# Optimization experiments

Measured on AMD Instinct MI355X. Metric: run time of the kernel, lower is better.

## Reference

```python
import jax, jax.numpy as jnp
import numpy as np

B, S, D, H, DK, F = 8, 1024, 1024, 16, 64, 4096
EPS = 1e-5


def _layer_norm(x, g, b):
    mu = jnp.mean(x, axis=-1, keepdims=True)
    var = jnp.var(x, axis=-1, keepdims=True)
    return (x - mu) * jax.lax.rsqrt(var + EPS) * g + b


def setup_inputs() -> dict:
    key = jax.random.key(0)
    ks = jax.random.split(key, 16)
    s = lambda fan: 1.0 / np.sqrt(fan)
    return {
        "src": jax.random.normal(ks[0], (B, S, D), dtype=jnp.float32),
        "Wq": jax.random.uniform(ks[1], (H, D, DK), jnp.float32, -s(D), s(D)),
        "bq": jnp.zeros((H, DK), jnp.float32),
        "Wk": jax.random.uniform(ks[2], (H, D, DK), jnp.float32, -s(D), s(D)),
        "bk": jnp.zeros((H, DK), jnp.float32),
        "Wv": jax.random.uniform(ks[3], (H, D, DK), jnp.float32, -s(D), s(D)),
        "bv": jnp.zeros((H, DK), jnp.float32),
        "Wo": jax.random.uniform(ks[4], (H * DK, D), jnp.float32, -s(H * DK), s(H * DK)),
        "bo": jnp.zeros((D,), jnp.float32),
        "g1": jnp.ones((D,), jnp.float32),
        "be1": jnp.zeros((D,), jnp.float32),
        "W1": jax.random.uniform(ks[5], (D, F), jnp.float32, -s(D), s(D)),
        "b1": jnp.zeros((F,), jnp.float32),
        "W2": jax.random.uniform(ks[6], (F, D), jnp.float32, -s(F), s(F)),
        "b2": jnp.zeros((D,), jnp.float32),
        "g2": jnp.ones((D,), jnp.float32),
        "be2": jnp.zeros((D,), jnp.float32),
    }


def reference(src, Wq, bq, Wk, bk, Wv, bv, Wo, bo, g1, be1, W1, b1, W2, b2, g2, be2):
    # Per-head projections (vectorized over the Python head loop of the original)
    q = jnp.einsum("bsd,hdk->bhsk", src, Wq) + bq[:, None, :]
    k = jnp.einsum("bsd,hdk->bhsk", src, Wk) + bk[:, None, :]
    v = jnp.einsum("bsd,hdk->bhsk", src, Wv) + bv[:, None, :]
    scale = 1.0 / jnp.sqrt(jnp.asarray(DK, src.dtype))
    scores = jnp.einsum("bhsk,bhtk->bhst", q, k) * scale  # [B,H,S,S]
    attn = jax.nn.softmax(scores, axis=-1)
    o = jnp.einsum("bhst,bhtk->bhsk", attn, v)
    # torch.cat over heads on last dim -> [B,S,H*DK] with head-major feature order
    o = o.transpose(0, 2, 1, 3).reshape(B, S, H * DK)
    attn_out = o @ Wo + bo
    x = _layer_norm(src + attn_out, g1, be1)  # dropout inactive at inference
    ff = jax.nn.relu(x @ W1 + b1) @ W2 + b2
    return _layer_norm(x + ff, g2, be2)
```

## Files before the change

### kernel.cpp

```cpp
#include <hip/hip_runtime.h>

#define Bq 8
#define Sq 1024
#define Dq 1024
#define Hq 16
#define DKq 64
#define Fq 4096
#define TOK (Bq*Sq)

typedef unsigned short u16;
typedef unsigned int u32;
typedef __bf16 bf16x8 __attribute__((ext_vector_type(8)));
typedef float  f32x4  __attribute__((ext_vector_type(4)));

__device__ __forceinline__ float bf2f(u16 u) {
  u32 x = ((u32)u) << 16;
  float f; __builtin_memcpy(&f, &x, 4); return f;
}
__device__ __forceinline__ u16 f2bf(float f) {
  u32 u; __builtin_memcpy(&u, &f, 4);
  u += 0x7fffu + ((u >> 16) & 1u);
  return (u16)(u >> 16);
}
__device__ __forceinline__ void async16(const u16* g, u16* l) {
  __builtin_amdgcn_global_load_lds(
      (__attribute__((address_space(1))) void*)(g),
      (__attribute__((address_space(3))) void*)(l), 16, 0, 0);
}
__device__ __forceinline__ u16 load_in(const void* p, long idx, u32 fp32) {
  return fp32 ? f2bf(((const float*)p)[idx]) : ((const u16*)p)[idx];
}

struct InTab { const void* p[17]; int n[17]; };

__global__ void detect_all(InTab tab, u32* flags) {
  __shared__ int sh[3][256];
  int bi = blockIdx.x;
  const u16* buf = (const u16*)tab.p[bi];
  long n = tab.n[bi];
  long m = n < 65536 ? n : 65536;
  int t = threadIdx.x;
  int nanpat = 0, evz = 0, oddnz = 0;
  for (long i = t; i < m; i += 256) {
    u16 v = buf[i];
    if ((v & 0x7F80u) == 0x7F80u) nanpat++;
    if ((i & 1) == 0) { if (v == 0) evz++; }
    else { if (v != 0) oddnz++; }
  }
  sh[0][t] = nanpat; sh[1][t] = evz; sh[2][t] = oddnz;
  __syncthreads();
  for (int s = 128; s > 0; s >>= 1) {
    if (t < s) { sh[0][t] += sh[0][t+s]; sh[1][t] += sh[1][t+s]; sh[2][t] += sh[2][t+s]; }
    __syncthreads();
  }
  if (t == 0) {
    long half = m / 2;
    bool fp32 = (sh[0][0] > 8) ||
                (sh[1][0] > (half * 9) / 10 && sh[2][0] > (half * 9) / 10);
    flags[bi] = fp32 ? 1u : 0u;
  }
}

__global__ void diag_ws_too_small(u16* out, float code) { out[0] = f2bf(code); }

__global__ void diag_mixed(const u32* flags, void* out) {
  u32 a = flags[0];
  if (flags[1] != a || flags[7] != a || flags[11] != a || flags[13] != a) {
    if (a) ((float*)out)[0] = 3000.0f;
    else ((u16*)out)[0] = f2bf(3000.0f);
  }
}

__global__ __launch_bounds__(256) void pack_all(const void* __restrict__ Wq,
                                                const void* __restrict__ Wk,
                                                const void* __restrict__ Wv,
                                                const void* __restrict__ Wo,
                                                const void* __restrict__ W1,
                                                const void* __restrict__ W2,
                                                u16* __restrict__ Wqkv_t,
                                                u16* __restrict__ Wo_t,
                                                u16* __restrict__ W1_t,
                                                u16* __restrict__ W2_t,
                                                const u32* __restrict__ flags) {
  int id = blockIdx.x;
  const void* in; u16* out; u32 f; int R, C; long zin; int r0, c0;
  if (id < 768) {
    int w = id >> 8, t = id & 255;
    int z = t >> 4, xt = t & 15;
    in = (w == 0) ? Wq : ((w == 1) ? Wk : Wv);
    f = flags[(w == 0) ? 1 : ((w == 1) ? 3 : 5)];
    R = 1024; C = 64;
    zin = (long)z * 65536;
    out = Wqkv_t + (long)w * 1048576 + (long)z * 65536;
    r0 = xt * 64; c0 = 0;
  } else if (id < 1024) {
    int t = id - 768; int xt = t & 15, yt = t >> 4;
    in = Wo; f = flags[7]; R = 1024; C = 1024; zin = 0; out = Wo_t;
    r0 = xt * 64; c0 = yt * 64;
  } else if (id < 2048) {
    int t = id - 1024; int xt = t & 15, yt = t >> 4;
    in = W1; f = flags[11]; R = 1024; C = 4096; zin = 0; out = W1_t;
    r0 = xt * 64; c0 = yt * 64;
  } else {
    int t = id - 2048; int xt = t & 63, yt = t >> 6;
    in = W2; f = flags[13]; R = 4096; C = 1024; zin = 0; out = W2_t;
    r0 = xt * 64; c0 = yt * 64;
  }
  __shared__ u16 tile[64][65];
  int tx = threadIdx.x & 63, ty = threadIdx.x >> 6;
#pragma unroll
  for (int it = 0; it < 16; it++) {
    int row = it * 4 + ty;
    tile[row][tx] = load_in(in, zin + (long)(r0 + row) * C + (c0 + tx), f);
  }
  __syncthreads();
#pragma unroll
  for (int it = 0; it < 16; it++) {
    int cc = it * 4 + ty;
    out[(long)(c0 + cc) * R + r0 + tx] = tile[tx][cc];
  }
}

struct CvtTab { const void* p[10]; int flagidx[10]; int dstoff[10]; int n[10]; };
__global__ void cvt_small(CvtTab tab, u16* __restrict__ dst, const u32* __restrict__ flags) {
  int e = blockIdx.x;
  u32 f = flags[tab.flagidx[e]];
  const void* p = tab.p[e];
  int n = tab.n[e], o = tab.dstoff[e];
  for (int i = threadIdx.x; i < n; i += 256) dst[o + i] = load_in(p, i, f);
}

__global__ __launch_bounds__(256) void cvt_src(const void* __restrict__ in,
                                               u16* __restrict__ out,
                                               const u32* __restrict__ flag) {
  u32 f = *flag;
  long i8 = ((long)blockIdx.x * 256 + threadIdx.x) * 8;
  if (f) {
    const float4* f4 = (const float4*)((const float*)in + i8);
    float4 a = f4[0], b = f4[1];
    u16 v[8] = {f2bf(a.x), f2bf(a.y), f2bf(a.z), f2bf(a.w),
                f2bf(b.x), f2bf(b.y), f2bf(b.z), f2bf(b.w)};
    *(uint4*)(out + i8) = *(const uint4*)v;
  } else {
    *(uint4*)(out + i8) = *(const uint4*)((const u16*)in + i8);
  }
}

__global__ __launch_bounds__(256) void gemm_bt(const u16* __restrict__ A,
                                               const u16* __restrict__ Bt,
                                               const u16* __restrict__ bias,
                                               u16* __restrict__ C,
                                               int M, int N, int K, int act) {
  __shared__ alignas(16) u16 sA[2][128 * 32];
  __shared__ alignas(16) u16 sB[2][128 * 32];
  const int tid = threadIdx.x;
  const int wv = tid >> 6, lane = tid & 63;
  const int m16 = lane & 15, quad = lane >> 4;
  const long bm = (long)blockIdx.x * 128;
  const long bn = (long)blockIdx.y * 128;
  const int wm = (wv >> 1) * 64, wn = (wv & 1) * 64;

  f32x4 acc[4][4];
#pragma unroll
  for (int i = 0; i < 4; i++)
#pragma unroll
    for (int j = 0; j < 4; j++) acc[i][j] = (f32x4){0.f, 0.f, 0.f, 0.f};

  const int row_s = tid >> 2;
  const int col_s = (tid & 3) * 8;
  const u16* gA0 = A + (bm + row_s) * (long)K + col_s;
  const u16* gA1 = gA0 + 64 * (long)K;
  const u16* gB0 = Bt + (bn + row_s) * (long)K + col_s;
  const u16* gB1 = gB0 + 64 * (long)K;

  auto stage = [&](int p, int k) {
    async16(gA0 + k, &sA[p][wv * 512]);
    async16(gA1 + k, &sA[p][2048 + wv * 512]);
    async16(gB0 + k, &sB[p][wv * 512]);
    async16(gB1 + k, &sB[p][2048 + wv * 512]);
  };
  auto compute = [&](int p) {
    bf16x8 af[4], bf_[4];
#pragma unroll
    for (int mi = 0; mi < 4; mi++)
      af[mi] = *(const bf16x8*)&sA[p][(wm + mi * 16 + m16) * 32 + quad * 8];
#pragma unroll
    for (int ni = 0; ni < 4; ni++)
      bf_[ni] = *(const bf16x8*)&sB[p][(wn + ni * 16 + m16) * 32 + quad * 8];
#pragma unroll
    for (int mi = 0; mi < 4; mi++)
#pragma unroll
      for (int ni = 0; ni < 4; ni++)
        acc[mi][ni] = __builtin_amdgcn_mfma_f32_16x16x32_bf16(af[mi], bf_[ni], acc[mi][ni], 0, 0, 0);
  };

  stage(0, 0);
  for (int k0 = 0; k0 < K; k0 += 64) {
    __syncthreads();
    if (k0 + 32 < K) stage(1, k0 + 32);
    compute(0);
    __syncthreads();
    if (k0 + 64 < K) stage(0, k0 + 64);
    compute(1);
  }

  float bv4[4];
#pragma unroll
  for (int ni = 0; ni < 4; ni++) bv4[ni] = bf2f(bias[bn + wn + ni * 16 + m16]);

#pragma unroll
  for (int mi = 0; mi < 4; mi++) {
#pragma unroll
    for (int ni = 0; ni < 4; ni++) {
      long col = bn + wn + ni * 16 + m16;
#pragma unroll
      for (int r = 0; r < 4; r++) {
        long row = bm + wm + mi * 16 + quad * 4 + r;
        float v = acc[mi][ni][r] + bv4[ni];
        if (act) v = fmaxf(v, 0.f);
        C[row * N + col] = f2bf(v);
      }
    }
  }
}

#define MF16 __builtin_amdgcn_mfma_f32_16x16x32_bf16

#define TILE256(BUF, NBUF, DOA, DOB, KA, KB, VMS)                              \
  {                                                                            \
                   \
    _Pragma("unroll") for (int mi = 0; mi < 4; mi++)                           \
      _Pragma("unroll") for (int kk = 0; kk < 2; kk++)                         \
        afr[mi][kk] = *(const bf16x8*)&sA[BUF][offA + mi * 1024 + kof[kk]];    \
    _Pragma("unroll") for (int ni = 0; ni < 2; ni++)                           \
      _Pragma("unroll") for (int kk = 0; kk < 2; kk++)                         \
        bfr[ni][kk] = *(const bf16x8*)&sB[BUF][offB + ni * 1024 + kof[kk]];    \
    if (DOA) stA(NBUF, 0, KA);                                                 \
    __builtin_amdgcn_s_barrier();                                              \
    __builtin_amdgcn_s_setprio(1);                                             \
    _Pragma("unroll") for (int kk = 0; kk < 2; kk++)                           \
      _Pragma("unroll") for (int mi = 0; mi < 4; mi++)                         \
        _Pragma("unroll") for (int ni = 0; ni < 2; ni++)                       \
          acc[mi][ni] = MF16(afr[mi][kk], bfr[ni][kk], acc[mi][ni], 0, 0, 0);  \
    __builtin_amdgcn_s_setprio(0);                                             \
    __builtin_amdgcn_s_barrier();                                              \
                                 \
    _Pragma("unroll") for (int ni = 0; ni < 2; ni++)                           \
      _Pragma("unroll") for (int kk = 0; kk < 2; kk++)                         \
        bfr[2 + ni][kk] = *(const bf16x8*)&sB[BUF][offB + (2 + ni) * 1024 + kof[kk]]; \
    if (DOA) stA(NBUF, 1, KA);                                                 \
    __builtin_amdgcn_s_barrier();                                              \
    __builtin_amdgcn_s_setprio(1);                                             \
    _Pragma("unroll") for (int kk = 0; kk < 2; kk++)                           \
      _Pragma("unroll") for (int mi = 0; mi < 4; mi++)                         \
        _Pragma("unroll") for (int ni = 0; ni < 2; ni++)                       \
          acc[mi][2 + ni] = MF16(afr[mi][kk], bfr[2 + ni][kk], acc[mi][2 + ni], 0, 0, 0); \
    __builtin_amdgcn_s_setprio(0);                                             \
    __builtin_amdgcn_s_barrier();                                              \
     \
    _Pragma("unroll") for (int mi = 0; mi < 4; mi++)                           \
      _Pragma("unroll") for (int kk = 0; kk < 2; kk++)                         \
        afr[mi][kk] = *(const bf16x8*)&sA[BUF][offA + (4 + mi) * 1024 + kof[kk]]; \
    if (DOB) stB(BUF, 0, KB);                                                  \
    __builtin_amdgcn_s_barrier();                                              \
    __builtin_amdgcn_s_setprio(1);                                             \
    _Pragma("unroll") for (int kk = 0; kk < 2; kk++)                           \
      _Pragma("unroll") for (int mi = 0; mi < 4; mi++)                         \
        _Pragma("unroll") for (int ni = 0; ni < 2; ni++)                       \
          acc[4 + mi][2 + ni] = MF16(afr[mi][kk], bfr[2 + ni][kk], acc[4 + mi][2 + ni], 0, 0, 0); \
    __builtin_amdgcn_s_setprio(0);                                             \
    __builtin_amdgcn_s_barrier();                                              \
           \
    if (DOB) stB(BUF, 1, KB);                                                  \
    asm volatile("s_waitcnt vmcnt(" VMS ")" ::: "memory");                     \
    __builtin_amdgcn_s_barrier();                                              \
    __builtin_amdgcn_s_setprio(1);                                             \
    _Pragma("unroll") for (int kk = 0; kk < 2; kk++)                           \
      _Pragma("unroll") for (int mi = 0; mi < 4; mi++)                         \
        _Pragma("unroll") for (int ni = 0; ni < 2; ni++)                       \
          acc[4 + mi][ni] = MF16(afr[mi][kk], bfr[ni][kk], acc[4 + mi][ni], 0, 0, 0); \
    __builtin_amdgcn_s_setprio(0);                                             \
    __builtin_amdgcn_s_barrier();                                              \
  }

__global__ __launch_bounds__(512, 2) void gemm256(const u16* __restrict__ A,
                                                  const u16* __restrict__ Bt,
                                                  const u16* __restrict__ bias,
                                                  u16* __restrict__ C,
                                                  int M, int N, int K, int act) {
  __shared__ alignas(16) u16 sA[2][16384];
  __shared__ alignas(16) u16 sB[2][16384];
  const int tid = threadIdx.x;
  const int wv = tid >> 6, lane = tid & 63;
  const int m16 = lane & 15, quad = lane >> 4;
  const int wr = wv >> 2, wc = wv & 3;

  const int NT = N >> 8;
  int bid = blockIdx.x;
  {
    const int nwg = gridDim.x;
    const int q = nwg >> 3, r = nwg & 7;
    const int xcd = bid & 7, lp = bid >> 3;
    bid = (xcd < r ? xcd * (q + 1) : r * (q + 1) + (xcd - r) * q) + lp;
  }
  const long bm = (long)(bid / NT) * 256;
  const long bn = (long)(bid % NT) * 256;

  const int r0 = wv * 16 + (lane >> 3);
  const int cstg = ((lane & 7) ^ (lane >> 3)) * 8;
  const u16* gA0 = A  + (bm + r0) * (long)K + cstg;
  const u16* gA1 = A  + (bm + 128 + r0) * (long)K + cstg;
  const u16* gB0 = Bt + (bn + r0) * (long)K + cstg;
  const u16* gB1 = Bt + (bn + 128 + r0) * (long)K + cstg;
  const long k8 = 8 * (long)K;

  auto stA = [&](int nb, int h, int k0) {
    const u16* s = (h ? gA1 : gA0) + k0;
    u16* d = &sA[nb][h * 8192 + wv * 1024];
    async16(s, d);
    async16(s + k8, d + 512);
  };
  auto stB = [&](int nb, int h, int k0) {
    const u16* s = (h ? gB1 : gB0) + k0;
    u16* d = &sB[nb][h * 8192 + wv * 1024];
    async16(s, d);
    async16(s + k8, d + 512);
  };

  const int qs = quad ^ (m16 & 3);
  const int hb = (m16 >> 2) & 1;
  const int kof[2] = {hb * 32, 32 - hb * 32};
  const int offA = wr * 8192 + m16 * 64 + qs * 8;
  const int offB = (wc >> 1) * 8192 + (wc & 1) * 4096 + m16 * 64 + qs * 8;

  f32x4 acc[8][4];
#pragma unroll
  for (int i = 0; i < 8; i++)
#pragma unroll
    for (int j = 0; j < 4; j++) acc[i][j] = (f32x4){0.f, 0.f, 0.f, 0.f};
  bf16x8 afr[4][2], bfr[4][2];

  const int KT = K >> 6;

  stA(0, 0, 0); stA(0, 1, 0); stB(0, 0, 0); stB(0, 1, 0);
  stB(1, 0, 64); stB(1, 1, 64);
  asm volatile("s_waitcnt vmcnt(4)" ::: "memory");
  __builtin_amdgcn_s_barrier();

  int T = 0;
  for (; T + 2 < KT; T += 2) {
    const int kA1 = (T + 1) << 6, kB2 = (T + 2) << 6, kB3 = (T + 3) << 6;
    TILE256(0, 1, true, true, kA1, kB2, "4");
    TILE256(1, 0, true, true, kB2, kB3, "4");
  }
  {
    const int kA1 = (T + 1) << 6;
    TILE256(0, 1, true, false, kA1, 0, "0");
    TILE256(1, 0, false, false, 0, 0, "0");
  }

  float bv4[4];
#pragma unroll
  for (int ni = 0; ni < 4; ni++) bv4[ni] = bf2f(bias[bn + wc * 64 + ni * 16 + m16]);

#pragma unroll
  for (int mi = 0; mi < 8; mi++) {
#pragma unroll
    for (int ni = 0; ni < 4; ni++) {
      long col = bn + wc * 64 + ni * 16 + m16;
      long rowb = bm + wr * 128 + mi * 16 + quad * 4;
#pragma unroll
      for (int r = 0; r < 4; r++) {
        float v = acc[mi][ni][r] + bv4[ni];
        if (act) v = fmaxf(v, 0.f);
        C[(rowb + r) * (long)N + col] = f2bf(v);
      }
    }
  }
}

__global__ __launch_bounds__(256, 3) void attn_fwd(const u16* __restrict__ qkv,
                                                   u16* __restrict__ attnO) {
  __shared__ alignas(16) u16 sQP[4608];
  __shared__ alignas(16) u16 sK[4608];
  __shared__ alignas(16) u16 sVt[4608];
  const int tid = threadIdx.x;
  const int bh = blockIdx.x;
  const int qt = blockIdx.y;
  const int b = bh >> 4, h = bh & 15;
  const int wv = tid >> 6, lane = tid & 63;
  const int m16 = lane & 15, quad = lane >> 4;
  const int toct = tid & 7;
  const int r_0 = tid >> 3;
  const int d_0 = (tid & 7) * 8;

#pragma unroll
  for (int i = 0; i < 2; i++) {
    int r = i * 32 + r_0;
    const u16* g = qkv + ((long)(b * Sq + qt * 64 + r)) * 3072 + h * 64 + d_0;
    uint4 raw = *(const uint4*)g;
    const u16* pv = (const u16*)&raw;
    u16 t[8];
#pragma unroll
    for (int j = 0; j < 8; j++) t[j] = f2bf(bf2f(pv[j]) * 0.125f);
    *(uint4*)&sQP[r * 72 + d_0] = *(const uint4*)t;
  }
  __syncthreads();
  bf16x8 aq0 = *(const bf16x8*)&sQP[(wv * 16 + m16) * 72 + quad * 8];
  bf16x8 aq1 = *(const bf16x8*)&sQP[(wv * 16 + m16) * 72 + 32 + quad * 8];

  f32x4 oacc[4];
#pragma unroll
  for (int ni = 0; ni < 4; ni++) oacc[ni] = (f32x4){0.f, 0.f, 0.f, 0.f};
  float mrun = -1e30f, lrun = 0.f;

  const u16* gK0 = qkv + (long)(b * Sq + r_0) * 3072 + h * 64 + d_0 + 1024;
  const u16* gK1 = gK0 + 32 * 3072;
  const long step = 64 * 3072;

  uint4 rk0 = *(const uint4*)gK0;
  uint4 rk1 = *(const uint4*)gK1;
  uint4 rv0 = *(const uint4*)(gK0 + 1024);
  uint4 rv1 = *(const uint4*)(gK1 + 1024);

  for (int kt = 0; kt < 16; kt++) {
    __syncthreads();
    *(uint4*)&sK[r_0 * 72 + d_0] = rk0;
    *(uint4*)&sK[(r_0 + 32) * 72 + d_0] = rk1;
    {
      const u16* pv0 = (const u16*)&rv0;
      const u16* pv1 = (const u16*)&rv1;
#pragma unroll
      for (int j = 0; j < 8; j++) {
        int jr = (j + toct) & 7;
        sVt[(d_0 + jr) * 72 + r_0] = pv0[jr];
        sVt[(d_0 + jr) * 72 + r_0 + 32] = pv1[jr];
      }
    }
    __syncthreads();

    if (kt < 15) {
      const u16* nK0 = gK0 + (long)(kt + 1) * step;
      const u16* nK1 = gK1 + (long)(kt + 1) * step;
      rk0 = *(const uint4*)nK0;
      rk1 = *(const uint4*)nK1;
      rv0 = *(const uint4*)(nK0 + 1024);
      rv1 = *(const uint4*)(nK1 + 1024);
    }

    f32x4 st[4];
#pragma unroll
    for (int ni = 0; ni < 4; ni++) st[ni] = (f32x4){0.f, 0.f, 0.f, 0.f};
    __builtin_amdgcn_s_setprio(1);
#pragma unroll
    for (int ni = 0; ni < 4; ni++) {
      bf16x8 bk0 = *(const bf16x8*)&sK[(ni * 16 + m16) * 72 + quad * 8];
      bf16x8 bk1 = *(const bf16x8*)&sK[(ni * 16 + m16) * 72 + 32 + quad * 8];
      st[ni] = __builtin_amdgcn_mfma_f32_16x16x32_bf16(bk0, aq0, st[ni], 0, 0, 0);
      st[ni] = __builtin_amdgcn_mfma_f32_16x16x32_bf16(bk1, aq1, st[ni], 0, 0, 0);
    }
    __builtin_amdgcn_s_setprio(0);

    float pmax = st[0][0];
#pragma unroll
    for (int ni = 0; ni < 4; ni++)
#pragma unroll
      for (int r = 0; r < 4; r++) pmax = fmaxf(pmax, st[ni][r]);
    pmax = fmaxf(pmax, __shfl_xor(pmax, 16));
    pmax = fmaxf(pmax, __shfl_xor(pmax, 32));
    float mnew = fmaxf(mrun, pmax);
    float alpha = __expf(mrun - mnew);
    mrun = mnew;

    u16* sPw = &sQP[wv * 1152];
    float rs = 0.f;
#pragma unroll
    for (int ni = 0; ni < 4; ni++) {
      u16 t4[4];
#pragma unroll
      for (int r = 0; r < 4; r++) {
        float p = __expf(st[ni][r] - mnew);
        rs += p;
        t4[r] = f2bf(p);
      }
      *(uint2*)&sPw[m16 * 72 + ni * 16 + quad * 4] = *(const uint2*)t4;
    }
    rs += __shfl_xor(rs, 16);
    rs += __shfl_xor(rs, 32);
    lrun = lrun * alpha + rs;
#pragma unroll
    for (int ni = 0; ni < 4; ni++)
#pragma unroll
      for (int r = 0; r < 4; r++) oacc[ni][r] *= alpha;

    bf16x8 pb0 = *(const bf16x8*)&sPw[m16 * 72 + quad * 8];
    bf16x8 pb1 = *(const bf16x8*)&sPw[m16 * 72 + 32 + quad * 8];

    __builtin_amdgcn_s_setprio(1);
#pragma unroll
    for (int ni = 0; ni < 4; ni++) {
      bf16x8 av0 = *(const bf16x8*)&sVt[(ni * 16 + m16) * 72 + quad * 8];
      bf16x8 av1 = *(const bf16x8*)&sVt[(ni * 16 + m16) * 72 + 32 + quad * 8];
      oacc[ni] = __builtin_amdgcn_mfma_f32_16x16x32_bf16(av0, pb0, oacc[ni], 0, 0, 0);
      oacc[ni] = __builtin_amdgcn_mfma_f32_16x16x32_bf16(av1, pb1, oacc[ni], 0, 0, 0);
    }
    __builtin_amdgcn_s_setprio(0);
  }

  float rl = 1.f / lrun;
  long row = (long)(b * Sq + qt * 64 + wv * 16 + m16);
#pragma unroll
  for (int ni = 0; ni < 4; ni++) {
    u16 t[4];
#pragma unroll
    for (int r = 0; r < 4; r++) t[r] = f2bf(oacc[ni][r] * rl);
    *(uint2*)&attnO[row * 1024 + h * 64 + ni * 16 + quad * 4] = *(const uint2*)t;
  }
}

__global__ __launch_bounds__(256) void add_ln(const u16* __restrict__ X,
                                              const u16* __restrict__ Y,
                                              const u16* __restrict__ g,
                                              const u16* __restrict__ be,
                                              u16* __restrict__ out) {
  const int row = blockIdx.x;
  const int t = threadIdx.x;
  const long base = (long)row * Dq;
  float v[4]; float s = 0.f, ss = 0.f;
#pragma unroll
  for (int i = 0; i < 4; i++) {
    int idx = i * 256 + t;
    float x = bf2f(X[base + idx]) + bf2f(Y[base + idx]);
    v[i] = x; s += x; ss += x * x;
  }
#pragma unroll
  for (int off = 32; off > 0; off >>= 1) { s += __shfl_down(s, off); ss += __shfl_down(ss, off); }
  __shared__ float red[8];
  int wv = t >> 6, ln = t & 63;
  if (ln == 0) { red[wv] = s; red[4 + wv] = ss; }
  __syncthreads();
  s = red[0] + red[1] + red[2] + red[3];
  ss = red[4] + red[5] + red[6] + red[7];
  float mean = s * (1.f / Dq);
  float var = ss * (1.f / Dq) - mean * mean;
  float rstd = rsqrtf(var + 1e-5f);
#pragma unroll
  for (int i = 0; i < 4; i++) {
    int idx = i * 256 + t;
    float o = (v[i] - mean) * rstd * bf2f(g[idx]) + bf2f(be[idx]);
    out[base + idx] = f2bf(o);
  }
}

__global__ __launch_bounds__(256) void add_ln_out(const u16* __restrict__ X,
                                                  const u16* __restrict__ Y,
                                                  const u16* __restrict__ g,
                                                  const u16* __restrict__ be,
                                                  void* __restrict__ out,
                                                  const u32* __restrict__ outflag) {
  const u32 fp32 = *outflag;
  const int row = blockIdx.x;
  const int t = threadIdx.x;
  const long base = (long)row * Dq;
  float v[4]; float s = 0.f, ss = 0.f;
#pragma unroll
  for (int i = 0; i < 4; i++) {
    int idx = i * 256 + t;
    float x = bf2f(X[base + idx]) + bf2f(Y[base + idx]);
    v[i] = x; s += x; ss += x * x;
  }
#pragma unroll
  for (int off = 32; off > 0; off >>= 1) { s += __shfl_down(s, off); ss += __shfl_down(ss, off); }
  __shared__ float red[8];
  int wv = t >> 6, ln = t & 63;
  if (ln == 0) { red[wv] = s; red[4 + wv] = ss; }
  __syncthreads();
  s = red[0] + red[1] + red[2] + red[3];
  ss = red[4] + red[5] + red[6] + red[7];
  float mean = s * (1.f / Dq);
  float var = ss * (1.f / Dq) - mean * mean;
  float rstd = rsqrtf(var + 1e-5f);
#pragma unroll
  for (int i = 0; i < 4; i++) {
    int idx = i * 256 + t;
    float o = (v[i] - mean) * rstd * bf2f(g[idx]) + bf2f(be[idx]);
    if (fp32) ((float*)out)[base + idx] = o;
    else ((u16*)out)[base + idx] = f2bf(o);
  }
}

extern "C" void kernel_launch(void* const* d_in, const int* in_sizes, int n_in,
                              void* d_out, int out_size, void* d_ws, size_t ws_size,
                              hipStream_t stream) {
  char* ws = (char*)d_ws;
  size_t off = 0;
  auto alloc = [&](size_t bytes) {
    void* p = ws + off;
    off += (bytes + 255) & ~(size_t)255;
    return p;
  };
  u32* flags  = (u32*)alloc(32 * 4);
  u16* Wqkv_t = (u16*)alloc((size_t)3072 * 1024 * 2);
  u16* Wo_t   = (u16*)alloc((size_t)1024 * 1024 * 2);
  u16* W1_t   = (u16*)alloc((size_t)4096 * 1024 * 2);
  u16* W2_t   = (u16*)alloc((size_t)1024 * 4096 * 2);
  u16* svec   = (u16*)alloc((size_t)13312 * 2);
  u16* src_bf = (u16*)alloc((size_t)TOK * 1024 * 2);
  u16* regA   = (u16*)alloc((size_t)TOK * 4096 * 2);
  size_t need_chunk2 = off;
  size_t need_full   = off + (size_t)TOK * 4096 * 2 / 2;

  u16* outw = (u16*)d_out;
  int CH;
  if (ws_size >= need_full) { CH = 8192; (void)alloc((size_t)32 << 20); }
  else if (ws_size >= need_chunk2) CH = 4096;
  else if (ws_size >= need_chunk2 - ((size_t)16 << 20)) CH = 2048;
  else {
    diag_ws_too_small<<<1, 1, 0, stream>>>(outw, 8000.0f + (float)(ws_size >> 20));
    return;
  }

  u16* qkv   = regA;
  u16* attnb = regA + (size_t)TOK * 3072;
  u16* proj  = regA;
  u16* x     = regA + (size_t)TOK * 1024;
  u16* h1    = regA + (size_t)TOK * 2048;
  u16* f2    = src_bf;

  u16* bqkv = svec + 0;
  u16* bo_c = svec + 3072;
  u16* g1_c = svec + 4096;
  u16* be1_c = svec + 5120;
  u16* b1_c = svec + 6144;
  u16* b2_c = svec + 10240;
  u16* g2_c = svec + 11264;
  u16* be2_c = svec + 12288;

  InTab itab;
  for (int i = 0; i < 17; i++) { itab.p[i] = d_in[i]; itab.n[i] = in_sizes[i]; }
  detect_all<<<dim3(17), 256, 0, stream>>>(itab, flags);

  pack_all<<<dim3(3072), 256, 0, stream>>>(d_in[1], d_in[3], d_in[5], d_in[7], d_in[11], d_in[13],
                                           Wqkv_t, Wo_t, W1_t, W2_t, flags);

  CvtTab ct;
  const int srcs[10] = {2, 4, 6, 8, 9, 10, 12, 14, 15, 16};
  const int offs[10] = {0, 1024, 2048, 3072, 4096, 5120, 6144, 10240, 11264, 12288};
  const int lens[10] = {1024, 1024, 1024, 1024, 1024, 1024, 4096, 1024, 1024, 1024};
  for (int e = 0; e < 10; e++) { ct.p[e] = d_in[srcs[e]]; ct.flagidx[e] = srcs[e]; ct.dstoff[e] = offs[e]; ct.n[e] = lens[e]; }
  cvt_small<<<dim3(10), 256, 0, stream>>>(ct, svec, flags);

  cvt_src<<<dim3(TOK * 1024 / (256 * 8)), 256, 0, stream>>>(d_in[0], src_bf, &flags[0]);

  gemm256<<<dim3(32 * 12), 512, 0, stream>>>(src_bf, Wqkv_t, bqkv, qkv, TOK, 3072, 1024, 0);
  attn_fwd<<<dim3(128, 16), 256, 0, stream>>>(qkv, attnb);
  gemm_bt<<<dim3(64, 8), 256, 0, stream>>>(attnb, Wo_t, bo_c, proj, TOK, 1024, 1024, 0);
  add_ln<<<dim3(TOK), 256, 0, stream>>>(src_bf, proj, g1_c, be1_c, x);
  for (int c = 0; c < TOK / CH; c++) {
    const u16* xc = x + (size_t)c * CH * 1024;
    u16* f2c = f2 + (size_t)c * CH * 1024;
    if (CH >= 4096) {
      gemm256<<<dim3((CH / 256) * 16), 512, 0, stream>>>(xc, W1_t, b1_c, h1, CH, 4096, 1024, 1);
    } else {
      gemm_bt<<<dim3(CH / 128, 32), 256, 0, stream>>>(xc, W1_t, b1_c, h1, CH, 4096, 1024, 1);
    }
    gemm_bt<<<dim3(CH / 128, 8), 256, 0, stream>>>(h1, W2_t, b2_c, f2c, CH, 1024, 4096, 0);
  }
  add_ln_out<<<dim3(TOK), 256, 0, stream>>>(x, f2, g2_c, be2_c, d_out, &flags[0]);
  diag_mixed<<<1, 1, 0, stream>>>(flags, d_out);
}
```

Before: 631.3 us.

## Write V transposed from QKV GEMM epilogue and widen attention query tile

The QKV GEMM epilogue now writes the V third directly in a per-head transposed [b,h,dk,s] layout, with Q/K kept in a 2048-wide buffer, so the attention kernel no longer transposes V element by element in shared memory. The attention kernel processes 128 query rows per block (32 per wave, two 16-row subtiles), reusing each K/V fragment load across two query tiles, and uses XOR-swizzled unpadded LDS layouts instead of padded rows. The trade-offs are scattered 8-byte stores of Vt in the GEMM epilogue, more registers per wave for the doubled accumulators, and half as many attention blocks.

Result: faster. 585.1 us (-7.3%).

```diff
diff --git a/kernel.cpp b/kernel.cpp
--- a/kernel.cpp
+++ b/kernel.cpp
@@ -29,6 +29,9 @@
 }
 __device__ __forceinline__ u16 load_in(const void* p, long idx, u32 fp32) {
   return fp32 ? f2bf(((const float*)p)[idx]) : ((const u16*)p)[idx];
+}
+__device__ __forceinline__ int swzb(int row, int colb) {
+  return row * 128 + (colb ^ ((row & 7) << 4));
 }
 
 struct InTab { const void* p[17]; int n[17]; };
@@ -287,7 +290,9 @@
                                                   const u16* __restrict__ Bt,
                                                   const u16* __restrict__ bias,
                                                   u16* __restrict__ C,
-                                                  int M, int N, int K, int act) {
+                                                  int M, int N, int K, int act,
+                                                  int ldc, u16* __restrict__ Vt,
+                                                  int mode) {
   __shared__ alignas(16) u16 sA[2][16384];
   __shared__ alignas(16) u16 sB[2][16384];
   const int tid = threadIdx.x;
@@ -369,152 +374,183 @@
     for (int ni = 0; ni < 4; ni++) {
       long col = bn + wc * 64 + ni * 16 + m16;
       long rowb = bm + wr * 128 + mi * 16 + quad * 4;
-#pragma unroll
-      for (int r = 0; r < 4; r++) {
-        float v = acc[mi][ni][r] + bv4[ni];
-        if (act) v = fmaxf(v, 0.f);
-        C[(rowb + r) * (long)N + col] = f2bf(v);
+      if (mode == 1 && col >= 2048) {
+        int hh = ((int)col >> 6) & 15, dk = (int)col & 63;
+        int bb = (int)(rowb >> 10), ss = (int)(rowb & 1023);
+        u16 t4[4];
+#pragma unroll
+        for (int r = 0; r < 4; r++) t4[r] = f2bf(acc[mi][ni][r] + bv4[ni]);
+        *(uint2*)&Vt[(((long)bb * 16 + hh) * 64 + dk) * 1024 + ss] = *(const uint2*)t4;
+      } else {
+#pragma unroll
+        for (int r = 0; r < 4; r++) {
+          float v = acc[mi][ni][r] + bv4[ni];
+          if (act) v = fmaxf(v, 0.f);
+          C[(rowb + r) * (long)ldc + col] = f2bf(v);
+        }
       }
     }
   }
 }
 
-__global__ __launch_bounds__(256, 3) void attn_fwd(const u16* __restrict__ qkv,
+__global__ __launch_bounds__(256, 4) void attn_fwd(const u16* __restrict__ qk,
+                                                   const u16* __restrict__ Vt,
                                                    u16* __restrict__ attnO) {
-  __shared__ alignas(16) u16 sQP[4608];
-  __shared__ alignas(16) u16 sK[4608];
-  __shared__ alignas(16) u16 sVt[4608];
+  __shared__ alignas(16) u16 sQP[8192];
+  __shared__ alignas(16) u16 sK[4096];
+  __shared__ alignas(16) u16 sVt[4096];
   const int tid = threadIdx.x;
   const int bh = blockIdx.x;
   const int qt = blockIdx.y;
   const int b = bh >> 4, h = bh & 15;
   const int wv = tid >> 6, lane = tid & 63;
   const int m16 = lane & 15, quad = lane >> 4;
-  const int toct = tid & 7;
-  const int r_0 = tid >> 3;
-  const int d_0 = (tid & 7) * 8;
-
-#pragma unroll
-  for (int i = 0; i < 2; i++) {
-    int r = i * 32 + r_0;
-    const u16* g = qkv + ((long)(b * Sq + qt * 64 + r)) * 3072 + h * 64 + d_0;
-    uint4 raw = *(const uint4*)g;
-    const u16* pv = (const u16*)&raw;
-    u16 t[8];
-#pragma unroll
-    for (int j = 0; j < 8; j++) t[j] = f2bf(bf2f(pv[j]) * 0.125f);
-    *(uint4*)&sQP[r * 72 + d_0] = *(const uint4*)t;
+  const int kk = tid >> 3;
+  const int t7 = tid & 7;
+
+  char* cQP = (char*)sQP;
+  char* cK = (char*)sK;
+  char* cV = (char*)sVt;
+
+  {
+    int row = tid >> 1, half = tid & 1;
+    const u16* g = qk + (long)(b * Sq + qt * 128 + row) * 2048 + h * 64 + half * 32;
+#pragma unroll
+    for (int j = 0; j < 4; j++) {
+      uint4 raw = *(const uint4*)(g + j * 8);
+      const u16* pv = (const u16*)&raw;
+      u16 t[8];
+#pragma unroll
+      for (int e = 0; e < 8; e++) t[e] = f2bf(bf2f(pv[e]) * 0.125f);
+      *(uint4*)(cQP + swzb(row, half * 64 + j * 16)) = *(const uint4*)t;
+    }
   }
   __syncthreads();
-  bf16x8 aq0 = *(const bf16x8*)&sQP[(wv * 16 + m16) * 72 + quad * 8];
-  bf16x8 aq1 = *(const bf16x8*)&sQP[(wv * 16 + m16) * 72 + 32 + quad * 8];
-
-  f32x4 oacc[4];
-#pragma unroll
-  for (int ni = 0; ni < 4; ni++) oacc[ni] = (f32x4){0.f, 0.f, 0.f, 0.f};
-  float mrun = -1e30f, lrun = 0.f;
-
-  const u16* gK0 = qkv + (long)(b * Sq + r_0) * 3072 + h * 64 + d_0 + 1024;
-  const u16* gK1 = gK0 + 32 * 3072;
-  const long step = 64 * 3072;
-
-  uint4 rk0 = *(const uint4*)gK0;
-  uint4 rk1 = *(const uint4*)gK1;
-  uint4 rv0 = *(const uint4*)(gK0 + 1024);
-  uint4 rv1 = *(const uint4*)(gK1 + 1024);
+  bf16x8 qf[2][2];
+#pragma unroll
+  for (int qt2 = 0; qt2 < 2; qt2++)
+#pragma unroll
+    for (int s = 0; s < 2; s++)
+      qf[qt2][s] = *(const bf16x8*)(cQP + swzb(wv * 32 + qt2 * 16 + m16, s * 64 + quad * 16));
+
+  f32x4 o[4][2];
+#pragma unroll
+  for (int dt = 0; dt < 4; dt++)
+#pragma unroll
+    for (int qt2 = 0; qt2 < 2; qt2++) o[dt][qt2] = (f32x4){0.f, 0.f, 0.f, 0.f};
+  float mrun[2] = {-1e30f, -1e30f}, lrun[2] = {0.f, 0.f};
+
+  const u16* gK = qk + (long)(b * Sq + kk) * 2048 + 1024 + h * 64 + t7 * 8;
+  const u16* gV = Vt + ((long)bh * 64 + kk) * 1024 + t7 * 8;
+  const long stepK = (long)64 * 2048;
+  const int off0 = swzb(kk, t7 * 16);
+  const int off1 = off0 + 4096;
+
+  uint4 rk0 = *(const uint4*)gK;
+  uint4 rk1 = *(const uint4*)(gK + 32 * 2048);
+  uint4 rv0 = *(const uint4*)gV;
+  uint4 rv1 = *(const uint4*)(gV + 32 * 1024);
 
   for (int kt = 0; kt < 16; kt++) {
     __syncthreads();
-    *(uint4*)&sK[r_0 * 72 + d_0] = rk0;
-    *(uint4*)&sK[(r_0 + 32) * 72 + d_0] = rk1;
-    {
-      const u16* pv0 = (const u16*)&rv0;
-      const u16* pv1 = (const u16*)&rv1;
-#pragma unroll
-      for (int j = 0; j < 8; j++) {
-        int jr = (j + toct) & 7;
-        sVt[(d_0 + jr) * 72 + r_0] = pv0[jr];
-        sVt[(d_0 + jr) * 72 + r_0 + 32] = pv1[jr];
+    *(uint4*)(cK + off0) = rk0;
+    *(uint4*)(cK + off1) = rk1;
+    *(uint4*)(cV + off0) = rv0;
+    *(uint4*)(cV + off1) = rv1;
+    __syncthreads();
+
+    f32x4 st[4][2];
+#pragma unroll
+    for (int kt2 = 0; kt2 < 4; kt2++)
+#pragma unroll
+      for (int qt2 = 0; qt2 < 2; qt2++) st[kt2][qt2] = (f32x4){0.f, 0.f, 0.f, 0.f};
+    __builtin_amdgcn_s_setprio(1);
+#pragma unroll
+    for (int s = 0; s < 2; s++) {
+      bf16x8 kf[4];
+#pragma unroll
+      for (int kt2 = 0; kt2 < 4; kt2++)
+        kf[kt2] = *(const bf16x8*)(cK + swzb(kt2 * 16 + m16, s * 64 + quad * 16));
+#pragma unroll
+      for (int kt2 = 0; kt2 < 4; kt2++)
+#pragma unroll
+        for (int qt2 = 0; qt2 < 2; qt2++)
+          st[kt2][qt2] = MF16(kf[kt2], qf[qt2][s], st[kt2][qt2], 0, 0, 0);
+    }
+    __builtin_amdgcn_s_setprio(0);
+
+    if (kt < 15) {
+      rk0 = *(const uint4*)(gK + (long)(kt + 1) * stepK);
+      rk1 = *(const uint4*)(gK + (long)(kt + 1) * stepK + 32 * 2048);
+      rv0 = *(const uint4*)(gV + (kt + 1) * 64);
+      rv1 = *(const uint4*)(gV + (kt + 1) * 64 + 32 * 1024);
+    }
+
+    char* cP = cQP + wv * 4096;
+#pragma unroll
+    for (int qt2 = 0; qt2 < 2; qt2++) {
+      float pm = st[0][qt2][0];
+#pragma unroll
+      for (int kt2 = 0; kt2 < 4; kt2++)
+#pragma unroll
+        for (int r = 0; r < 4; r++) pm = fmaxf(pm, st[kt2][qt2][r]);
+      pm = fmaxf(pm, __shfl_xor(pm, 16));
+      pm = fmaxf(pm, __shfl_xor(pm, 32));
+      float mnew = fmaxf(mrun[qt2], pm);
+      float al = __expf(mrun[qt2] - mnew);
+      mrun[qt2] = mnew;
+      float rs = 0.f;
+#pragma unroll
+      for (int kt2 = 0; kt2 < 4; kt2++) {
+        u16 t4[4];
+#pragma unroll
+        for (int r = 0; r < 4; r++) {
+          float p = __expf(st[kt2][qt2][r] - mnew);
+          rs += p;
+          t4[r] = f2bf(p);
+        }
+        *(uint2*)(cP + swzb(qt2 * 16 + m16, kt2 * 32 + quad * 8)) = *(const uint2*)t4;
       }
-    }
-    __syncthreads();
-
-    if (kt < 15) {
-      const u16* nK0 = gK0 + (long)(kt + 1) * step;
-      const u16* nK1 = gK1 + (long)(kt + 1) * step;
-      rk0 = *(const uint4*)nK0;
-      rk1 = *(const uint4*)nK1;
-      rv0 = *(const uint4*)(nK0 + 1024);
-      rv1 = *(const uint4*)(nK1 + 1024);
-    }
-
-    f32x4 st[4];
-#pragma unroll
-    for (int ni = 0; ni < 4; ni++) st[ni] = (f32x4){0.f, 0.f, 0.f, 0.f};
+      rs += __shfl_xor(rs, 16);
+      rs += __shfl_xor(rs, 32);
+      lrun[qt2] = lrun[qt2] * al + rs;
+#pragma unroll
+      for (int dt = 0; dt < 4; dt++)
+#pragma unroll
+        for (int r = 0; r < 4; r++) o[dt][qt2][r] *= al;
+    }
+
+    bf16x8 pb[2][2];
+#pragma unroll
+    for (int qt2 = 0; qt2 < 2; qt2++)
+#pragma unroll
+      for (int ks = 0; ks < 2; ks++)
+        pb[qt2][ks] = *(const bf16x8*)(cP + swzb(qt2 * 16 + m16, ks * 64 + quad * 16));
     __builtin_amdgcn_s_setprio(1);
 #pragma unroll
-    for (int ni = 0; ni < 4; ni++) {
-      bf16x8 bk0 = *(const bf16x8*)&sK[(ni * 16 + m16) * 72 + quad * 8];
-      bf16x8 bk1 = *(const bf16x8*)&sK[(ni * 16 + m16) * 72 + 32 + quad * 8];
-      st[ni] = __builtin_amdgcn_mfma_f32_16x16x32_bf16(bk0, aq0, st[ni], 0, 0, 0);
-      st[ni] = __builtin_amdgcn_mfma_f32_16x16x32_bf16(bk1, aq1, st[ni], 0, 0, 0);
+    for (int dt = 0; dt < 4; dt++) {
+      bf16x8 v0 = *(const bf16x8*)(cV + swzb(dt * 16 + m16, quad * 16));
+      bf16x8 v1 = *(const bf16x8*)(cV + swzb(dt * 16 + m16, 64 + quad * 16));
+#pragma unroll
+      for (int qt2 = 0; qt2 < 2; qt2++) {
+        o[dt][qt2] = MF16(v0, pb[qt2][0], o[dt][qt2], 0, 0, 0);
+        o[dt][qt2] = MF16(v1, pb[qt2][1], o[dt][qt2], 0, 0, 0);
+      }
     }
     __builtin_amdgcn_s_setprio(0);
-
-    float pmax = st[0][0];
-#pragma unroll
-    for (int ni = 0; ni < 4; ni++)
-#pragma unroll
-      for (int r = 0; r < 4; r++) pmax = fmaxf(pmax, st[ni][r]);
-    pmax = fmaxf(pmax, __shfl_xor(pmax, 16));
-    pmax = fmaxf(pmax, __shfl_xor(pmax, 32));
-    float mnew = fmaxf(mrun, pmax);
-    float alpha = __expf(mrun - mnew);
-    mrun = mnew;
-
-    u16* sPw = &sQP[wv * 1152];
-    float rs = 0.f;
-#pragma unroll
-    for (int ni = 0; ni < 4; ni++) {
+  }
+
+#pragma unroll
+  for (int qt2 = 0; qt2 < 2; qt2++) {
+    float rl = 1.f / lrun[qt2];
+    long tok = (long)(b * Sq + qt * 128 + wv * 32 + qt2 * 16 + m16);
+#pragma unroll
+    for (int dt = 0; dt < 4; dt++) {
       u16 t4[4];
 #pragma unroll
-      for (int r = 0; r < 4; r++) {
-        float p = __expf(st[ni][r] - mnew);
-        rs += p;
-        t4[r] = f2bf(p);
-      }
-      *(uint2*)&sPw[m16 * 72 + ni * 16 + quad * 4] = *(const uint2*)t4;
-    }
-    rs += __shfl_xor(rs, 16);
-    rs += __shfl_xor(rs, 32);
-    lrun = lrun * alpha + rs;
-#pragma unroll
-    for (int ni = 0; ni < 4; ni++)
-#pragma unroll
-      for (int r = 0; r < 4; r++) oacc[ni][r] *= alpha;
-
-    bf16x8 pb0 = *(const bf16x8*)&sPw[m16 * 72 + quad * 8];
-    bf16x8 pb1 = *(const bf16x8*)&sPw[m16 * 72 + 32 + quad * 8];
-
-    __builtin_amdgcn_s_setprio(1);
-#pragma unroll
-    for (int ni = 0; ni < 4; ni++) {
-      bf16x8 av0 = *(const bf16x8*)&sVt[(ni * 16 + m16) * 72 + quad * 8];
-      bf16x8 av1 = *(const bf16x8*)&sVt[(ni * 16 + m16) * 72 + 32 + quad * 8];
-      oacc[ni] = __builtin_amdgcn_mfma_f32_16x16x32_bf16(av0, pb0, oacc[ni], 0, 0, 0);
-      oacc[ni] = __builtin_amdgcn_mfma_f32_16x16x32_bf16(av1, pb1, oacc[ni], 0, 0, 0);
-    }
-    __builtin_amdgcn_s_setprio(0);
-  }
-
-  float rl = 1.f / lrun;
-  long row = (long)(b * Sq + qt * 64 + wv * 16 + m16);
-#pragma unroll
-  for (int ni = 0; ni < 4; ni++) {
-    u16 t[4];
-#pragma unroll
-    for (int r = 0; r < 4; r++) t[r] = f2bf(oacc[ni][r] * rl);
-    *(uint2*)&attnO[row * 1024 + h * 64 + ni * 16 + quad * 4] = *(const uint2*)t;
+      for (int r = 0; r < 4; r++) t4[r] = f2bf(o[dt][qt2][r] * rl);
+      *(uint2*)&attnO[tok * 1024 + h * 64 + dt * 16 + quad * 4] = *(const uint2*)t4;
+    }
   }
 }
 
@@ -620,7 +656,8 @@
     return;
   }
 
-  u16* qkv   = regA;
+  u16* qk    = regA;
+  u16* Vt    = regA + (size_t)TOK * 2048;
   u16* attnb = regA + (size_t)TOK * 3072;
   u16* proj  = regA;
   u16* x     = regA + (size_t)TOK * 1024;
@@ -652,15 +689,17 @@
 
   cvt_src<<<dim3(TOK * 1024 / (256 * 8)), 256, 0, stream>>>(d_in[0], src_bf, &flags[0]);
 
-  gemm256<<<dim3(32 * 12), 512, 0, stream>>>(src_bf, Wqkv_t, bqkv, qkv, TOK, 3072, 1024, 0);
-  attn_fwd<<<dim3(128, 16), 256, 0, stream>>>(qkv, attnb);
+  gemm256<<<dim3(32 * 12), 512, 0, stream>>>(src_bf, Wqkv_t, bqkv, qk, TOK, 3072, 1024, 0,
+                                             2048, Vt, 1);
+  attn_fwd<<<dim3(128, 8), 256, 0, stream>>>(qk, Vt, attnb);
   gemm_bt<<<dim3(64, 8), 256, 0, stream>>>(attnb, Wo_t, bo_c, proj, TOK, 1024, 1024, 0);
   add_ln<<<dim3(TOK), 256, 0, stream>>>(src_bf, proj, g1_c, be1_c, x);
   for (int c = 0; c < TOK / CH; c++) {
     const u16* xc = x + (size_t)c * CH * 1024;
     u16* f2c = f2 + (size_t)c * CH * 1024;
     if (CH >= 4096) {
-      gemm256<<<dim3((CH / 256) * 16), 512, 0, stream>>>(xc, W1_t, b1_c, h1, CH, 4096, 1024, 1);
+      gemm256<<<dim3((CH / 256) * 16), 512, 0, stream>>>(xc, W1_t, b1_c, h1, CH, 4096, 1024, 1,
+                                                         4096, nullptr, 0);
     } else {
       gemm_bt<<<dim3(CH / 128, 32), 256, 0, stream>>>(xc, W1_t, b1_c, h1, CH, 4096, 1024, 1);
     }
```
